# Kernel optimization log

Hardware: AMD Instinct MI355X
Metric: run time of the kernel (lower is better)

Reference implementation:

```python
import jax, jax.numpy as jnp
import numpy as np

B, S, H, NH, HD = 2, 2048, 1024, 16, 64
RD = 16            # rotary_dim = head_dim * 0.25
W = 16             # mini_context_length (sliding window)
SCALE = HD ** -0.5
ROPE_BASE = 10000.0


def setup_inputs() -> dict:
    key = jax.random.key(0)
    ks = jax.random.split(key, 10)
    p = lambda k, shape: (jax.random.normal(k, shape, dtype=jnp.float32) * 0.02)
    return {
        "hidden_states": jax.random.normal(ks[0], (B, S, H), dtype=jnp.float32),
        "Wqkv": p(ks[1], (3 * H, H)), "bqkv": p(ks[2], (3 * H,)),
        "Wqa": p(ks[3], (H, H)),      "bqa": p(ks[4], (H,)),
        "Wka": p(ks[5], (H, H)),      "bka": p(ks[6], (H,)),
        "Wd": p(ks[7], (H, H)),       "bd": p(ks[8], (H,)),
    }


def _rotate_half(x):
    x1, x2 = jnp.split(x, 2, axis=-1)
    return jnp.concatenate([-x2, x1], axis=-1)


def _apply_rope(q, k, seq_len):
    # GPT-NeoX style rotary on the first RD dims. q,k: [B,NH,S,RD]
    inv_freq = 1.0 / (ROPE_BASE ** (jnp.arange(0, RD, 2, dtype=jnp.float32) / RD))
    t = jnp.arange(seq_len, dtype=jnp.float32)
    freqs = jnp.outer(t, inv_freq)                     # [S, RD//2]
    emb = jnp.concatenate([freqs, freqs], axis=-1)     # [S, RD]
    cos = jnp.cos(emb)[None, None]                      # [1,1,S,RD]
    sin = jnp.sin(emb)[None, None]
    return q * cos + _rotate_half(q) * sin, k * cos + _rotate_half(k) * sin


def reference(hidden_states, Wqkv, bqkv, Wqa, bqa, Wka, bka, Wd, bd):
    b, s, _ = hidden_states.shape
    qkv = hidden_states @ Wqkv.T + bqkv                       # [B,S,3H]
    qkv = qkv.reshape(b, s, 3, NH, HD).transpose(2, 0, 3, 1, 4)
    q, k, v = qkv[0], qkv[1], qkv[2]                          # [B,NH,S,HD]

    q_rot, k_rot = _apply_rope(q[..., :RD], k[..., :RD], s)
    q = jnp.concatenate([q_rot, q[..., RD:]], axis=-1)
    k = jnp.concatenate([k_rot, k[..., RD:]], axis=-1)

    # ----- Stage 1: sliding-window local attention (vectorized) -----
    pos = jnp.arange(s)
    idx = pos[:, None] - (W - 1) + jnp.arange(W)[None, :]     # [S,W]
    valid = idx >= 0
    idxc = jnp.clip(idx, 0, s - 1)
    k_win = k[:, :, idxc, :]                                   # [B,NH,S,W,HD]
    v_win = v[:, :, idxc, :]
    scores = jnp.einsum('bhsd,bhswd->bhsw', q, k_win) * SCALE
    scores = jnp.where(valid[None, None], scores, -jnp.inf)
    probs = jax.nn.softmax(scores, axis=-1)
    A = jnp.einsum('bhsw,bhswd->bhsd', probs, v_win)           # [B,NH,S,HD]

    A_hidden = A.transpose(0, 2, 1, 3).reshape(b, s, H)        # [B,S,H]

    # ----- Stage 2: causal global attention over A -----
    qa = (A_hidden @ Wqa.T + bqa).reshape(b, s, NH, HD).transpose(0, 2, 1, 3)
    ka = (A_hidden @ Wka.T + bka).reshape(b, s, NH, HD).transpose(0, 2, 1, 3)
    g = jnp.einsum('bhqd,bhkd->bhqk', qa, ka) * SCALE          # [B,NH,S,S]
    causal = pos[:, None] >= pos[None, :]
    g = jnp.where(causal[None, None], g, -jnp.inf)
    pg = jax.nn.softmax(g, axis=-1)
    out = jnp.einsum('bhqk,bhkd->bhqd', pg, A)                 # [B,NH,S,HD]
    out = out.transpose(0, 2, 1, 3).reshape(b, s, H)
    return out @ Wd.T + bd
```

## Files before the change

### kernel.cpp

```cpp
#include <hip/hip_runtime.h>
#include <hip/hip_bf16.h>
#include <cstdint>
#include <cstddef>

typedef __bf16 bf16;
typedef __bf16 bf16x4 __attribute__((ext_vector_type(4)));
typedef __bf16 bf16x8 __attribute__((ext_vector_type(8)));
typedef float  f32x4  __attribute__((ext_vector_type(4)));

#define DEVINL __device__ __forceinline__

constexpr int   Bc  = 2, Sc = 2048, Hc = 1024, NHc = 16, HDc = 64;
constexpr int   Tc  = Bc * Sc;
constexpr float L2E = 1.44269504088896340736f;
constexpr float NEG_BIG = -1.0e30f;

typedef __attribute__((address_space(1))) void AS1void;
typedef __attribute__((address_space(3))) void AS3void;

DEVINL void load_lds16(const bf16* g, bf16* l) {
  __builtin_amdgcn_global_load_lds((AS1void*)g, (AS3void*)l, 16, 0, 0);
}


__global__ __launch_bounds__(256)
void convert_all(const float* __restrict__ hs, const float* __restrict__ Wqkv,
                 const float* __restrict__ Wqa, const float* __restrict__ Wka,
                 const float* __restrict__ Wd, const float* __restrict__ bqa,
                 const float* __restrict__ bka,
                 bf16* __restrict__ hsb, bf16* __restrict__ wqkvb,
                 bf16* __restrict__ wqakab, bf16* __restrict__ wdb,
                 float* __restrict__ bqaka) {
  const int blk = blockIdx.x;
  if (blk >= 5120) {
    const int i = threadIdx.x * 8;
    const float* src = (i < 1024) ? (bqa + i) : (bka + i - 1024);
    *(f32x4*)(bqaka + i)     = *(const f32x4*)src;
    *(f32x4*)(bqaka + i + 4) = *(const f32x4*)(src + 4);
    return;
  }
  const float* src; bf16* dst; int base;
  if      (blk < 2048) { src = hs;   dst = hsb;                    base = blk; }
  else if (blk < 3584) { src = Wqkv; dst = wqkvb;                  base = blk - 2048; }
  else if (blk < 4096) { src = Wqa;  dst = wqakab;                 base = blk - 3584; }
  else if (blk < 4608) { src = Wka;  dst = wqakab + 1024 * 1024;   base = blk - 4096; }
  else                 { src = Wd;   dst = wdb;                    base = blk - 4608; }
  const int i = (base * 256 + threadIdx.x) * 8;
  f32x4 a = *(const f32x4*)(src + i);
  f32x4 b = *(const f32x4*)(src + i + 4);
  bf16x8 v;
#pragma unroll
  for (int j = 0; j < 4; j++) { v[j] = (bf16)a[j]; v[4 + j] = (bf16)b[j]; }
  *(bf16x8*)(dst + i) = v;
}

template <typename CT>
__global__ __launch_bounds__(256, 3)
void gemm128(const bf16* __restrict__ A, const bf16* __restrict__ Bw,
             const float* __restrict__ bias, CT* __restrict__ C,
             int M, int N, int K) {
  __shared__ __attribute__((aligned(16))) bf16 As[128 * 64];
  __shared__ __attribute__((aligned(16))) bf16 Bs[128 * 64];

  const int tid = threadIdx.x, wv = tid >> 6, lane = tid & 63;
  const int m0 = blockIdx.y * 128, n0 = blockIdx.x * 128;
  const int col = lane & 15, quad = lane >> 4;
  const int wrow = (wv >> 1) * 64, wcol = (wv & 1) * 64;

  f32x4 acc[4][4];
#pragma unroll
  for (int i = 0; i < 4; i++)
#pragma unroll
    for (int j = 0; j < 4; j++) acc[i][j] = f32x4{0.f, 0.f, 0.f, 0.f};

  const int srow = tid >> 3;
  const int scol = (((tid & 7) ^ (srow & 7)) << 3);
  const bf16* Ag = A  + (size_t)(m0 + srow) * K + scol;
  const bf16* Bg = Bw + (size_t)(n0 + srow) * K + scol;
  const int cs = col & 7;

  for (int k0 = 0; k0 < K; k0 += 64) {
#pragma unroll
    for (int c = 0; c < 4; c++) {
      load_lds16(Ag + (size_t)(c * 32) * K + k0, As + c * 2048 + tid * 8);
      load_lds16(Bg + (size_t)(c * 32) * K + k0, Bs + c * 2048 + tid * 8);
    }
    __syncthreads();
#pragma unroll
    for (int kk = 0; kk < 64; kk += 32) {
      const int so = ((((kk >> 3) + quad) ^ cs) << 3);
      bf16x8 af[4], bfr[4];
#pragma unroll
      for (int i = 0; i < 4; i++)
        af[i] = *(const bf16x8*)(As + (wrow + i * 16 + col) * 64 + so);
#pragma unroll
      for (int j = 0; j < 4; j++)
        bfr[j] = *(const bf16x8*)(Bs + (wcol + j * 16 + col) * 64 + so);
#pragma unroll
      for (int i = 0; i < 4; i++)
#pragma unroll
        for (int j = 0; j < 4; j++)
          acc[i][j] = __builtin_amdgcn_mfma_f32_16x16x32_bf16(af[i], bfr[j], acc[i][j], 0, 0, 0);
    }
    __syncthreads();
  }

#pragma unroll
  for (int j = 0; j < 4; j++) {
    const int c = n0 + wcol + j * 16 + col;
    const float bv = bias[c];
#pragma unroll
    for (int i = 0; i < 4; i++)
#pragma unroll
      for (int r = 0; r < 4; r++) {
        const int rr = m0 + wrow + i * 16 + quad * 4 + r;
        C[(size_t)rr * N + c] = (CT)(acc[i][j][r] + bv);
      }
  }
}

template <typename CT>
__global__ __launch_bounds__(256, 4)
void gemm6464(const bf16* __restrict__ A, const bf16* __restrict__ Bw,
              const float* __restrict__ bias, CT* __restrict__ C,
              int M, int N, int K) {
  __shared__ __attribute__((aligned(16))) bf16 As[64 * 64];
  __shared__ __attribute__((aligned(16))) bf16 Bs[64 * 64];

  const int tid = threadIdx.x, wv = tid >> 6, lane = tid & 63;
  const int m0 = blockIdx.y * 64, n0 = blockIdx.x * 64;
  const int col = lane & 15, quad = lane >> 4;

  f32x4 acc[4];
#pragma unroll
  for (int j = 0; j < 4; j++) acc[j] = f32x4{0.f, 0.f, 0.f, 0.f};

  const int srow = tid >> 3;
  const int scol = (((tid & 7) ^ (srow & 7)) << 3);
  const bf16* Ag = A  + (size_t)(m0 + srow) * K + scol;
  const bf16* Bg = Bw + (size_t)(n0 + srow) * K + scol;
  const int cs = col & 7;

  for (int k0 = 0; k0 < K; k0 += 64) {
#pragma unroll
    for (int c = 0; c < 2; c++) {
      load_lds16(Ag + (size_t)(c * 32) * K + k0, As + c * 2048 + tid * 8);
      load_lds16(Bg + (size_t)(c * 32) * K + k0, Bs + c * 2048 + tid * 8);
    }
    __syncthreads();
#pragma unroll
    for (int kk = 0; kk < 64; kk += 32) {
      const int so = ((((kk >> 3) + quad) ^ cs) << 3);
      bf16x8 af = *(const bf16x8*)(As + (wv * 16 + col) * 64 + so);
#pragma unroll
      for (int j = 0; j < 4; j++) {
        bf16x8 bfr = *(const bf16x8*)(Bs + (j * 16 + col) * 64 + so);
        acc[j] = __builtin_amdgcn_mfma_f32_16x16x32_bf16(af, bfr, acc[j], 0, 0, 0);
      }
    }
    __syncthreads();
  }

#pragma unroll
  for (int j = 0; j < 4; j++) {
    const int c = n0 + j * 16 + col;
    const float bv = bias[c];
#pragma unroll
    for (int r = 0; r < 4; r++) {
      const int rr = m0 + wv * 16 + quad * 4 + r;
      C[(size_t)rr * N + c] = (CT)(acc[j][r] + bv);
    }
  }
}

__global__ __launch_bounds__(256)
void window_attn(const bf16* __restrict__ qkv, bf16* __restrict__ Ah,
                 bf16* __restrict__ VTg) {
  __shared__ __attribute__((aligned(16))) bf16 Kw[31 * 72];
  __shared__ __attribute__((aligned(16))) bf16 Vw[31 * 72];
  const int g  = blockIdx.x;
  const int st = g & 127;
  const int h  = (g >> 7) & 15;
  const int b  = g >> 11;
  const int s0 = st * 16;
  const int tid = threadIdx.x;

  if ((tid < 124) || (tid >= 128 && tid < 252)) {
    const bool isK = tid < 124;
    const int lt  = isK ? tid : tid - 128;
    const int r   = lt >> 2, off = (lt & 3) << 4;
    int sidx = s0 - 15 + r; if (sidx < 0) sidx = 0;
    const bf16* src = qkv + (size_t)(b * Sc + sidx) * 3072 + (isK ? 1024 : 2048) + h * 64 + off;
    bf16x8 v0 = *(const bf16x8*)src;
    bf16x8 v1 = *(const bf16x8*)(src + 8);
    if (isK && off == 0) {
#pragma unroll
      for (int j = 0; j < 8; j++) {
        const float invf = exp2f(-(float)j * 1.66096404744368128f);
        float sn, csn;
        sincosf((float)sidx * invf, &sn, &csn);
        const float x1 = (float)v0[j], x2 = (float)v1[j];
        v0[j] = (bf16)(x1 * csn - x2 * sn);
        v1[j] = (bf16)(x2 * csn + x1 * sn);
      }
    }
    bf16* dst = (isK ? Kw : Vw) + r * 72 + off;
    *(bf16x8*)dst       = v0;
    *(bf16x8*)(dst + 8) = v1;
  }
  __syncthreads();

  const int wv = tid >> 6, lane = tid & 63;
  const int subq = lane >> 4, lane16 = lane & 15;
  const int s = s0 + wv * 4 + subq;
  const int t = b * Sc + s;
  const int d0 = lane16 * 4;

  float qd[4];
  {
    bf16x4 qv = *(const bf16x4*)(qkv + (size_t)t * 3072 + h * 64 + d0);
#pragma unroll
    for (int j = 0; j < 4; j++) qd[j] = (float)qv[j];
  }
  float pd[4];
#pragma unroll
  for (int j = 0; j < 4; j++) pd[j] = __shfl_xor(qd[j], 2, 64);
  if (lane16 < 4) {
#pragma unroll
    for (int j = 0; j < 4; j++) {
      const int jabs = d0 + j;
      const float invf = exp2f(-(float)(jabs & 7) * 1.66096404744368128f);
      float sn, csn;
      sincosf((float)s * invf, &sn, &csn);
      qd[j] = (jabs < 8) ? (qd[j] * csn - pd[j] * sn) : (qd[j] * csn + pd[j] * sn);
    }
  }

  float sc[16];
#pragma unroll
  for (int w = 0; w < 16; w++) {
    const int idxp = s - 15 + w;
    const int row = idxp - s0 + 15;
    bf16x4 kv = *(const bf16x4*)(Kw + row * 72 + d0);
    float p = qd[0] * (float)kv[0] + qd[1] * (float)kv[1] +
              qd[2] * (float)kv[2] + qd[3] * (float)kv[3];
#pragma unroll
    for (int m = 1; m < 16; m <<= 1) p += __shfl_xor(p, m, 64);
    sc[w] = (idxp < 0) ? NEG_BIG : p * 0.125f;
  }
  float mx = sc[0];
#pragma unroll
  for (int w = 1; w < 16; w++) mx = fmaxf(mx, sc[w]);
  float sum = 0.f;
#pragma unroll
  for (int w = 0; w < 16; w++) { sc[w] = exp2f((sc[w] - mx) * L2E); sum += sc[w]; }
  const float inv = 1.0f / fmaxf(sum, 1e-30f);

  float acc[4] = {0.f, 0.f, 0.f, 0.f};
#pragma unroll
  for (int w = 0; w < 16; w++) {
    const int idxp = s - 15 + w;
    const int row = idxp - s0 + 15;
    bf16x4 vv = *(const bf16x4*)(Vw + row * 72 + d0);
#pragma unroll
    for (int j = 0; j < 4; j++) acc[j] += sc[w] * (float)vv[j];
  }
  bf16x4 ov;
#pragma unroll
  for (int j = 0; j < 4; j++) ov[j] = (bf16)(acc[j] * inv);
  *(bf16x4*)(Ah + (size_t)t * 1024 + h * 64 + d0) = ov;
  bf16* vt = VTg + (((size_t)(b * 16 + h)) * 64 + d0) * 2048 + s;
#pragma unroll
  for (int j = 0; j < 4; j++) vt[(size_t)j * 2048] = ov[j];
}

__global__ __launch_bounds__(256, 2)
void flash_attn(const bf16* __restrict__ Q, const bf16* __restrict__ Kt,
                const bf16* __restrict__ VTg, bf16* __restrict__ O) {
  constexpr int QS = 2048;
  constexpr float SHIFT = 16.0f;
  __shared__ __attribute__((aligned(16))) bf16 K_lds[2][128 * 64];
  __shared__ __attribute__((aligned(16))) bf16 VT_lds[2][64 * 128];

  const int tid = threadIdx.x, wv = tid >> 6, lane = tid & 63;
  const int bh = blockIdx.x;
  const int y  = blockIdx.y;
  const int qtA = y, qtB = 31 - y;
  const int nA = (qtA + 2) >> 1;
  const int b = bh >> 4, h = bh & 15;
  const int col = lane & 15, quad = lane >> 4;
  const size_t bS = (size_t)b * Sc;
  const int hd = h * 64;

  const int krow = tid >> 3;
  const int kcol = (((tid & 7) ^ (krow & 7)) << 3);
  const int vrow = tid >> 4;
  const int vcol = (((tid & 15) ^ vrow) << 3);
  const int cs8 = col & 7;

  bf16x8 qA0, qA1, qB0, qB1;
  {
    const bf16* qpA = Q + (bS + qtA * 64 + wv * 16 + col) * QS + hd + quad * 8;
    const bf16* qpB = Q + (bS + qtB * 64 + wv * 16 + col) * QS + hd + quad * 8;
    qA0 = *(const bf16x8*)qpA;
    qA1 = *(const bf16x8*)(qpA + 32);
    qB0 = *(const bf16x8*)qpB;
    qB1 = *(const bf16x8*)(qpB + 32);
#pragma unroll
    for (int j = 0; j < 8; j++) {
      qA0[j] = (bf16)((float)qA0[j] * 0.125f);
      qA1[j] = (bf16)((float)qA1[j] * 0.125f);
      qB0[j] = (bf16)((float)qB0[j] * 0.125f);
      qB1[j] = (bf16)((float)qB1[j] * 0.125f);
    }
  }

  auto stage = [&](int bufi, int k0) {
#pragma unroll
    for (int c = 0; c < 4; c++) {
      load_lds16(Kt + (bS + k0 + c * 32 + krow) * QS + hd + kcol,
                 K_lds[bufi] + c * 2048 + tid * 8);
      load_lds16(VTg + ((size_t)bh * 64 + c * 16 + vrow) * 2048 + k0 + vcol,
                 VT_lds[bufi] + c * 2048 + tid * 8);
    }
  };

  f32x4 oacc[4];
#pragma unroll
  for (int i = 0; i < 4; i++) oacc[i] = f32x4{0.f, 0.f, 0.f, 0.f};
  float lsum = 0.f;

  stage(0, 0);
  __syncthreads();
  int cur = 0;

  for (int it = 0; it < 17; it++) {
    const int seg  = (it >= nA);
    const int kt   = seg ? (it - nA) : it;
    const int nkt  = seg ? (17 - nA) : nA;
    const int qt   = seg ? qtB : qtA;
    const int k0   = kt * 128;
    const int qbase = qt * 64 + wv * 16;

    if (it + 1 < 17) {
      const int kt2 = (it + 1 >= nA) ? (it + 1 - nA) : (it + 1);
      stage(cur ^ 1, kt2 * 128);
    }

    bf16x8 q0, q1;
    if (seg == 0) { q0 = qA0; q1 = qA1; } else { q0 = qB0; q1 = qB1; }

    const bf16* Kl = K_lds[cur];
    const bf16* Vl = VT_lds[cur];

    f32x4 sacc[8];
#pragma unroll
    for (int sub = 0; sub < 8; sub++) {
      f32x4 a = f32x4{0.f, 0.f, 0.f, 0.f};
      {
        const int so = ((quad ^ cs8) << 3);
        bf16x8 kf = *(const bf16x8*)(Kl + (sub * 16 + col) * 64 + so);
        a = __builtin_amdgcn_mfma_f32_16x16x32_bf16(kf, q0, a, 0, 0, 0);
      }
      {
        const int so = (((4 + quad) ^ cs8) << 3);
        bf16x8 kf = *(const bf16x8*)(Kl + (sub * 16 + col) * 64 + so);
        a = __builtin_amdgcn_mfma_f32_16x16x32_bf16(kf, q1, a, 0, 0, 0);
      }
      sacc[sub] = a;
    }
    if (kt == nkt - 1) {
      const int qq = qbase + col;
#pragma unroll
      for (int sub = 0; sub < 8; sub++)
#pragma unroll
        for (int r = 0; r < 4; r++) {
          const int key = k0 + sub * 16 + quad * 4 + r;
          if (key > qq) sacc[sub][r] = NEG_BIG;
        }
    }
#pragma unroll
    for (int sub = 0; sub < 8; sub++)
#pragma unroll
      for (int r = 0; r < 4; r++) {
        sacc[sub][r] = exp2f(sacc[sub][r] * L2E - SHIFT);
        lsum += sacc[sub][r];
      }

#pragma unroll
    for (int t = 0; t < 4; t++) {
      uint32_t a0, a1, b0, b1;
      asm("v_cvt_pk_bf16_f32 %0, %1, %2"
          : "=v"(a0) : "v"(sacc[2 * t][0]), "v"(sacc[2 * t][1]));
      asm("v_cvt_pk_bf16_f32 %0, %1, %2"
          : "=v"(a1) : "v"(sacc[2 * t][2]), "v"(sacc[2 * t][3]));
      asm("v_cvt_pk_bf16_f32 %0, %1, %2"
          : "=v"(b0) : "v"(sacc[2 * t + 1][0]), "v"(sacc[2 * t + 1][1]));
      asm("v_cvt_pk_bf16_f32 %0, %1, %2"
          : "=v"(b1) : "v"(sacc[2 * t + 1][2]), "v"(sacc[2 * t + 1][3]));
      asm("v_permlane32_swap_b32 %0, %1" : "+v"(a0), "+v"(b0));
      asm("v_permlane16_swap_b32 %0, %1" : "+v"(a0), "+v"(b0));
      asm("v_permlane32_swap_b32 %0, %1" : "+v"(a1), "+v"(b1));
      asm("v_permlane16_swap_b32 %0, %1" : "+v"(a1), "+v"(b1));
      union { uint32_t u[4]; bf16x8 v; } pk;
      pk.u[0] = a0; pk.u[1] = a1; pk.u[2] = b0; pk.u[3] = b1;
      const int vso = (((4 * t + quad) ^ col) << 3);
#pragma unroll
      for (int nb = 0; nb < 4; nb++) {
        bf16x8 vf = *(const bf16x8*)(Vl + (nb * 16 + col) * 128 + vso);
        oacc[nb] = __builtin_amdgcn_mfma_f32_16x16x32_bf16(pk.v, vf, oacc[nb], 0, 0, 0);
      }
    }

    if (kt == nkt - 1) {
      float tot = lsum;
      tot += __shfl_xor(tot, 16, 64);
      tot += __shfl_xor(tot, 32, 64);
      float lrow[4];
#pragma unroll
      for (int r = 0; r < 4; r++)
        lrow[r] = 1.0f / fmaxf(__shfl(tot, quad * 4 + r, 16), 1e-37f);
#pragma unroll
      for (int nb = 0; nb < 4; nb++)
#pragma unroll
        for (int r = 0; r < 4; r++) {
          const int qq = qbase + quad * 4 + r;
          O[(bS + qq) * 1024 + hd + nb * 16 + col] = (bf16)(oacc[nb][r] * lrow[r]);
        }
#pragma unroll
      for (int i = 0; i < 4; i++) oacc[i] = f32x4{0.f, 0.f, 0.f, 0.f};
      lsum = 0.f;
    }

    __syncthreads();
    cur ^= 1;
  }
}

extern "C" void kernel_launch(void* const* d_in, const int* in_sizes, int n_in,
                              void* d_out, int out_size, void* d_ws, size_t ws_size,
                              hipStream_t stream) {
  (void)in_sizes; (void)n_in; (void)out_size; (void)ws_size;
  const float* hs   = (const float*)d_in[0];
  const float* Wqkv = (const float*)d_in[1];
  const float* bqkv = (const float*)d_in[2];
  const float* Wqa  = (const float*)d_in[3];
  const float* bqa  = (const float*)d_in[4];
  const float* Wka  = (const float*)d_in[5];
  const float* bka  = (const float*)d_in[6];
  const float* Wd   = (const float*)d_in[7];
  const float* bd   = (const float*)d_in[8];
  float* out = (float*)d_out;

  const size_t TH = (size_t)Tc * Hc;
  bf16* dob   = (bf16*)d_out;
  bf16* hsb   = dob;
  bf16* wqkvb = dob + TH;
  bf16* Ah    = dob;
  bf16* VTg   = dob + TH;
  bf16* ws     = (bf16*)d_ws;
  bf16* qkv    = ws;
  bf16* qaka   = ws;
  bf16* oh     = ws + 2 * TH;
  bf16* wqakab = ws + 3 * TH;
  bf16* wdb    = wqakab + 2 * 1024 * 1024;
  float* bqaka = (float*)(wdb + 1024 * 1024);

  convert_all<<<dim3(5121), 256, 0, stream>>>(hs, Wqkv, Wqa, Wka, Wd, bqa, bka,
                                              hsb, wqkvb, wqakab, wdb, bqaka);

  gemm128<bf16><<<dim3(24, 32), 256, 0, stream>>>(hsb, wqkvb, bqkv, qkv, Tc, 3 * Hc, Hc);
  window_attn<<<dim3(Tc * NHc / 16), 256, 0, stream>>>(qkv, Ah, VTg);
  gemm128<bf16><<<dim3(16, 32), 256, 0, stream>>>(Ah, wqakab, bqaka, qaka, Tc, 2 * Hc, Hc);
  flash_attn<<<dim3(Bc * NHc, 16), 256, 0, stream>>>(qaka, qaka + Hc, VTg, oh);
  gemm6464<float><<<dim3(16, 64), 256, 0, stream>>>(oh, wdb, bd, out, Tc, Hc, Hc);
}
```

Baseline: 238.2 us.

## Split key tile across wave pairs in flash attention with LDS reduction

```diff
diff --git a/kernel.cpp b/kernel.cpp
--- a/kernel.cpp
+++ b/kernel.cpp
@@ -274,7 +274,7 @@
   for (int j = 0; j < 4; j++) vt[(size_t)j * 2048] = ov[j];
 }
 
-__global__ __launch_bounds__(256, 2)
+__global__ __launch_bounds__(512, 4)
 void flash_attn(const bf16* __restrict__ Q, const bf16* __restrict__ Kt,
                 const bf16* __restrict__ VTg, bf16* __restrict__ O) {
   constexpr int QS = 2048;
@@ -283,6 +283,7 @@
   __shared__ __attribute__((aligned(16))) bf16 VT_lds[2][64 * 128];
 
   const int tid = threadIdx.x, wv = tid >> 6, lane = tid & 63;
+  const int kw = wv & 1, qw = wv >> 1;
   const int bh = blockIdx.x;
   const int y  = blockIdx.y;
   const int qtA = y, qtB = 31 - y;
@@ -295,13 +296,13 @@
   const int krow = tid >> 3;
   const int kcol = (((tid & 7) ^ (krow & 7)) << 3);
   const int vrow = tid >> 4;
-  const int vcol = (((tid & 15) ^ vrow) << 3);
+  const int vcol = (((tid & 15) ^ (vrow & 15)) << 3);
   const int cs8 = col & 7;
 
   bf16x8 qA0, qA1, qB0, qB1;
   {
-    const bf16* qpA = Q + (bS + qtA * 64 + wv * 16 + col) * QS + hd + quad * 8;
-    const bf16* qpB = Q + (bS + qtB * 64 + wv * 16 + col) * QS + hd + quad * 8;
+    const bf16* qpA = Q + (bS + qtA * 64 + qw * 16 + col) * QS + hd + quad * 8;
+    const bf16* qpB = Q + (bS + qtB * 64 + qw * 16 + col) * QS + hd + quad * 8;
     qA0 = *(const bf16x8*)qpA;
     qA1 = *(const bf16x8*)(qpA + 32);
     qB0 = *(const bf16x8*)qpB;
@@ -317,11 +318,11 @@
 
   auto stage = [&](int bufi, int k0) {
 #pragma unroll
-    for (int c = 0; c < 4; c++) {
-      load_lds16(Kt + (bS + k0 + c * 32 + krow) * QS + hd + kcol,
-                 K_lds[bufi] + c * 2048 + tid * 8);
-      load_lds16(VTg + ((size_t)bh * 64 + c * 16 + vrow) * 2048 + k0 + vcol,
-                 VT_lds[bufi] + c * 2048 + tid * 8);
+    for (int c = 0; c < 2; c++) {
+      load_lds16(Kt + (bS + k0 + c * 64 + krow) * QS + hd + kcol,
+                 K_lds[bufi] + c * 4096 + tid * 8);
+      load_lds16(VTg + ((size_t)bh * 64 + c * 32 + vrow) * 2048 + k0 + vcol,
+                 VT_lds[bufi] + c * 4096 + tid * 8);
     }
   };
 
@@ -340,7 +341,7 @@
     const int nkt  = seg ? (17 - nA) : nA;
     const int qt   = seg ? qtB : qtA;
     const int k0   = kt * 128;
-    const int qbase = qt * 64 + wv * 16;
+    const int qbase = qt * 64 + qw * 16;
 
     if (it + 1 < 17) {
       const int kt2 = (it + 1 >= nA) ? (it + 1 - nA) : (it + 1);
@@ -350,12 +351,12 @@
     bf16x8 q0, q1;
     if (seg == 0) { q0 = qA0; q1 = qA1; } else { q0 = qB0; q1 = qB1; }
 
-    const bf16* Kl = K_lds[cur];
+    const bf16* Kl = K_lds[cur] + kw * 4096;
     const bf16* Vl = VT_lds[cur];
 
-    f32x4 sacc[8];
-#pragma unroll
-    for (int sub = 0; sub < 8; sub++) {
+    f32x4 sacc[4];
+#pragma unroll
+    for (int sub = 0; sub < 4; sub++) {
       f32x4 a = f32x4{0.f, 0.f, 0.f, 0.f};
       {
         const int so = ((quad ^ cs8) << 3);
@@ -372,15 +373,15 @@
     if (kt == nkt - 1) {
       const int qq = qbase + col;
 #pragma unroll
-      for (int sub = 0; sub < 8; sub++)
+      for (int sub = 0; sub < 4; sub++)
 #pragma unroll
         for (int r = 0; r < 4; r++) {
-          const int key = k0 + sub * 16 + quad * 4 + r;
+          const int key = k0 + kw * 64 + sub * 16 + quad * 4 + r;
           if (key > qq) sacc[sub][r] = NEG_BIG;
         }
     }
 #pragma unroll
-    for (int sub = 0; sub < 8; sub++)
+    for (int sub = 0; sub < 4; sub++)
 #pragma unroll
       for (int r = 0; r < 4; r++) {
         sacc[sub][r] = exp2f(sacc[sub][r] * L2E - SHIFT);
@@ -388,7 +389,7 @@
       }
 
 #pragma unroll
-    for (int t = 0; t < 4; t++) {
+    for (int t = 0; t < 2; t++) {
       uint32_t a0, a1, b0, b1;
       asm("v_cvt_pk_bf16_f32 %0, %1, %2"
           : "=v"(a0) : "v"(sacc[2 * t][0]), "v"(sacc[2 * t][1]));
@@ -404,7 +405,7 @@
       asm("v_permlane16_swap_b32 %0, %1" : "+v"(a1), "+v"(b1));
       union { uint32_t u[4]; bf16x8 v; } pk;
       pk.u[0] = a0; pk.u[1] = a1; pk.u[2] = b0; pk.u[3] = b1;
-      const int vso = (((4 * t + quad) ^ col) << 3);
+      const int vso = (((8 * kw + 4 * t + quad) ^ col) << 3);
 #pragma unroll
       for (int nb = 0; nb < 4; nb++) {
         bf16x8 vf = *(const bf16x8*)(Vl + (nb * 16 + col) * 128 + vso);
@@ -413,20 +414,37 @@
     }
 
     if (kt == nkt - 1) {
-      float tot = lsum;
-      tot += __shfl_xor(tot, 16, 64);
-      tot += __shfl_xor(tot, 32, 64);
-      float lrow[4];
-#pragma unroll
-      for (int r = 0; r < 4; r++)
-        lrow[r] = 1.0f / fmaxf(__shfl(tot, quad * 4 + r, 16), 1e-37f);
-#pragma unroll
-      for (int nb = 0; nb < 4; nb++)
-#pragma unroll
-        for (int r = 0; r < 4; r++) {
-          const int qq = qbase + quad * 4 + r;
-          O[(bS + qq) * 1024 + hd + nb * 16 + col] = (bf16)(oacc[nb][r] * lrow[r]);
-        }
+      __syncthreads();
+      float* scr = (qw < 2) ? (float*)(&K_lds[cur][0]) + ((qw * 64) + lane) * 17
+                            : (float*)(&VT_lds[cur][0]) + (((qw - 2) * 64) + lane) * 17;
+      if (kw == 1) {
+#pragma unroll
+        for (int nb = 0; nb < 4; nb++)
+#pragma unroll
+          for (int r = 0; r < 4; r++) scr[nb * 4 + r] = oacc[nb][r];
+        scr[16] = lsum;
+      }
+      __syncthreads();
+      if (kw == 0) {
+#pragma unroll
+        for (int nb = 0; nb < 4; nb++)
+#pragma unroll
+          for (int r = 0; r < 4; r++) oacc[nb][r] += scr[nb * 4 + r];
+        float tot = lsum + scr[16];
+        tot += __shfl_xor(tot, 16, 64);
+        tot += __shfl_xor(tot, 32, 64);
+        float lrow[4];
+#pragma unroll
+        for (int r = 0; r < 4; r++)
+          lrow[r] = 1.0f / fmaxf(__shfl(tot, quad * 4 + r, 16), 1e-37f);
+#pragma unroll
+        for (int nb = 0; nb < 4; nb++)
+#pragma unroll
+          for (int r = 0; r < 4; r++) {
+            const int qq = qbase + quad * 4 + r;
+            O[(bS + qq) * 1024 + hd + nb * 16 + col] = (bf16)(oacc[nb][r] * lrow[r]);
+          }
+      }
 #pragma unroll
       for (int i = 0; i < 4; i++) oacc[i] = f32x4{0.f, 0.f, 0.f, 0.f};
       lsum = 0.f;
@@ -472,6 +490,6 @@
   gemm128<bf16><<<dim3(24, 32), 256, 0, stream>>>(hsb, wqkvb, bqkv, qkv, Tc, 3 * Hc, Hc);
   window_attn<<<dim3(Tc * NHc / 16), 256, 0, stream>>>(qkv, Ah, VTg);
   gemm128<bf16><<<dim3(16, 32), 256, 0, stream>>>(Ah, wqakab, bqaka, qaka, Tc, 2 * Hc, Hc);
-  flash_attn<<<dim3(Bc * NHc, 16), 256, 0, stream>>>(qaka, qaka + Hc, VTg, oh);
+  flash_attn<<<dim3(Bc * NHc, 16), 512, 0, stream>>>(qaka, qaka + Hc, VTg, oh);
   gemm6464<float><<<dim3(16, 64), 256, 0, stream>>>(oh, wdb, bd, out, Tc, Hc, Hc);
 }
```

Result: no change. 238.9 us (+0.3%).

## Triple-buffer flash attention with 512-thread blocks and 128-row query tiles

Applied to the files above, without the earlier changes.

```diff
diff --git a/kernel.cpp b/kernel.cpp
--- a/kernel.cpp
+++ b/kernel.cpp
@@ -21,6 +21,12 @@
 DEVINL void load_lds16(const bf16* g, bf16* l) {
   __builtin_amdgcn_global_load_lds((AS1void*)g, (AS3void*)l, 16, 0, 0);
 }
+
+#if __has_builtin(__builtin_amdgcn_exp2f)
+DEVINL float fast_exp2(float x) { return __builtin_amdgcn_exp2f(x); }
+#else
+DEVINL float fast_exp2(float x) { return exp2f(x); }
+#endif
 
 
 __global__ __launch_bounds__(256)
@@ -274,56 +280,59 @@
   for (int j = 0; j < 4; j++) vt[(size_t)j * 2048] = ov[j];
 }
 
-__global__ __launch_bounds__(256, 2)
+__global__ __launch_bounds__(512, 2)
 void flash_attn(const bf16* __restrict__ Q, const bf16* __restrict__ Kt,
                 const bf16* __restrict__ VTg, bf16* __restrict__ O) {
   constexpr int QS = 2048;
-  constexpr float SHIFT = 16.0f;
-  __shared__ __attribute__((aligned(16))) bf16 K_lds[2][128 * 64];
-  __shared__ __attribute__((aligned(16))) bf16 VT_lds[2][64 * 128];
+  __shared__ __attribute__((aligned(16))) bf16 K_lds[3][128 * 64];
+  __shared__ __attribute__((aligned(16))) bf16 VT_lds[3][64 * 128];
 
   const int tid = threadIdx.x, wv = tid >> 6, lane = tid & 63;
   const int bh = blockIdx.x;
   const int y  = blockIdx.y;
-  const int qtA = y, qtB = 31 - y;
-  const int nA = (qtA + 2) >> 1;
+  const int qtA = y, qtB = 15 - y;
+  const int nA = y + 1;
   const int b = bh >> 4, h = bh & 15;
   const int col = lane & 15, quad = lane >> 4;
   const size_t bS = (size_t)b * Sc;
   const int hd = h * 64;
+  const int cs8 = col & 7;
 
   const int krow = tid >> 3;
-  const int kcol = (((tid & 7) ^ (krow & 7)) << 3);
+  const int kswz = (((tid & 7) ^ (krow & 7)) << 3);
   const int vrow = tid >> 4;
-  const int vcol = (((tid & 15) ^ vrow) << 3);
-  const int cs8 = col & 7;
+  const int vswz = (((tid & 15) ^ (vrow & 15)) << 3);
+  const bf16* Kg0 = Kt  + (bS * QS) + (size_t)krow * QS + hd + kswz;
+  const bf16* Vg0 = VTg + ((size_t)bh * 64 + vrow) * 2048 + vswz;
 
   bf16x8 qA0, qA1, qB0, qB1;
   {
-    const bf16* qpA = Q + (bS + qtA * 64 + wv * 16 + col) * QS + hd + quad * 8;
-    const bf16* qpB = Q + (bS + qtB * 64 + wv * 16 + col) * QS + hd + quad * 8;
+    constexpr float QSC = 0.125f * L2E;
+    const bf16* qpA = Q + (bS + qtA * 128 + wv * 16 + col) * QS + hd + quad * 8;
+    const bf16* qpB = Q + (bS + qtB * 128 + wv * 16 + col) * QS + hd + quad * 8;
     qA0 = *(const bf16x8*)qpA;
     qA1 = *(const bf16x8*)(qpA + 32);
     qB0 = *(const bf16x8*)qpB;
     qB1 = *(const bf16x8*)(qpB + 32);
 #pragma unroll
     for (int j = 0; j < 8; j++) {
-      qA0[j] = (bf16)((float)qA0[j] * 0.125f);
-      qA1[j] = (bf16)((float)qA1[j] * 0.125f);
-      qB0[j] = (bf16)((float)qB0[j] * 0.125f);
-      qB1[j] = (bf16)((float)qB1[j] * 0.125f);
+      qA0[j] = (bf16)((float)qA0[j] * QSC);
+      qA1[j] = (bf16)((float)qA1[j] * QSC);
+      qB0[j] = (bf16)((float)qB0[j] * QSC);
+      qB1[j] = (bf16)((float)qB1[j] * QSC);
     }
   }
 
   auto stage = [&](int bufi, int k0) {
-#pragma unroll
-    for (int c = 0; c < 4; c++) {
-      load_lds16(Kt + (bS + k0 + c * 32 + krow) * QS + hd + kcol,
-                 K_lds[bufi] + c * 2048 + tid * 8);
-      load_lds16(VTg + ((size_t)bh * 64 + c * 16 + vrow) * 2048 + k0 + vcol,
-                 VT_lds[bufi] + c * 2048 + tid * 8);
+    const bf16* kg = Kg0 + (size_t)k0 * QS;
+    const bf16* vg = Vg0 + k0;
+#pragma unroll
+    for (int c = 0; c < 2; c++) {
+      load_lds16(kg + (size_t)(c * 64) * QS, K_lds[bufi] + c * 4096 + tid * 8);
+      load_lds16(vg + (size_t)(c * 32) * 2048, VT_lds[bufi] + c * 4096 + tid * 8);
     }
   };
+  auto k0of = [&](int i) { return ((i >= nA) ? i - nA : i) * 128; };
 
   f32x4 oacc[4];
 #pragma unroll
@@ -331,8 +340,7 @@
   float lsum = 0.f;
 
   stage(0, 0);
-  __syncthreads();
-  int cur = 0;
+  stage(1, k0of(1));
 
   for (int it = 0; it < 17; it++) {
     const int seg  = (it >= nA);
@@ -340,20 +348,25 @@
     const int nkt  = seg ? (17 - nA) : nA;
     const int qt   = seg ? qtB : qtA;
     const int k0   = kt * 128;
-    const int qbase = qt * 64 + wv * 16;
-
-    if (it + 1 < 17) {
-      const int kt2 = (it + 1 >= nA) ? (it + 1 - nA) : (it + 1);
-      stage(cur ^ 1, kt2 * 128);
-    }
+    const int qbase = qt * 128 + wv * 16;
+    const int bufc = it % 3;
+
+    if (it == 16)                      asm volatile("s_waitcnt vmcnt(0)" ::: "memory");
+    else if (it == nA || it == nA + 1) asm volatile("s_waitcnt vmcnt(20)" ::: "memory");
+    else                               asm volatile("s_waitcnt vmcnt(4)" ::: "memory");
+    __builtin_amdgcn_s_barrier();
+    __builtin_amdgcn_sched_barrier(0);
+
+    if (it + 2 < 17) stage((it + 2) % 3, k0of(it + 2));
 
     bf16x8 q0, q1;
-    if (seg == 0) { q0 = qA0; q1 = qA1; } else { q0 = qB0; q1 = qB1; }
-
-    const bf16* Kl = K_lds[cur];
-    const bf16* Vl = VT_lds[cur];
+    if (seg) { q0 = qB0; q1 = qB1; } else { q0 = qA0; q1 = qA1; }
+
+    const bf16* Kl = K_lds[bufc];
+    const bf16* Vl = VT_lds[bufc];
 
     f32x4 sacc[8];
+    __builtin_amdgcn_s_setprio(1);
 #pragma unroll
     for (int sub = 0; sub < 8; sub++) {
       f32x4 a = f32x4{0.f, 0.f, 0.f, 0.f};
@@ -369,6 +382,8 @@
       }
       sacc[sub] = a;
     }
+    __builtin_amdgcn_s_setprio(0);
+
     if (kt == nkt - 1) {
       const int qq = qbase + col;
 #pragma unroll
@@ -383,8 +398,9 @@
     for (int sub = 0; sub < 8; sub++)
 #pragma unroll
       for (int r = 0; r < 4; r++) {
-        sacc[sub][r] = exp2f(sacc[sub][r] * L2E - SHIFT);
-        lsum += sacc[sub][r];
+        const float p = fast_exp2(sacc[sub][r]);
+        sacc[sub][r] = p;
+        lsum += p;
       }
 
 #pragma unroll
@@ -405,11 +421,13 @@
       union { uint32_t u[4]; bf16x8 v; } pk;
       pk.u[0] = a0; pk.u[1] = a1; pk.u[2] = b0; pk.u[3] = b1;
       const int vso = (((4 * t + quad) ^ col) << 3);
+      __builtin_amdgcn_s_setprio(1);
 #pragma unroll
       for (int nb = 0; nb < 4; nb++) {
         bf16x8 vf = *(const bf16x8*)(Vl + (nb * 16 + col) * 128 + vso);
         oacc[nb] = __builtin_amdgcn_mfma_f32_16x16x32_bf16(pk.v, vf, oacc[nb], 0, 0, 0);
       }
+      __builtin_amdgcn_s_setprio(0);
     }
 
     if (kt == nkt - 1) {
@@ -431,9 +449,6 @@
       for (int i = 0; i < 4; i++) oacc[i] = f32x4{0.f, 0.f, 0.f, 0.f};
       lsum = 0.f;
     }
-
-    __syncthreads();
-    cur ^= 1;
   }
 }
 
@@ -472,6 +487,6 @@
   gemm128<bf16><<<dim3(24, 32), 256, 0, stream>>>(hsb, wqkvb, bqkv, qkv, Tc, 3 * Hc, Hc);
   window_attn<<<dim3(Tc * NHc / 16), 256, 0, stream>>>(qkv, Ah, VTg);
   gemm128<bf16><<<dim3(16, 32), 256, 0, stream>>>(Ah, wqakab, bqaka, qaka, Tc, 2 * Hc, Hc);
-  flash_attn<<<dim3(Bc * NHc, 16), 256, 0, stream>>>(qaka, qaka + Hc, VTg, oh);
+  flash_attn<<<dim3(Bc * NHc, 8), 512, 0, stream>>>(qaka, qaka + Hc, VTg, oh);
   gemm6464<float><<<dim3(16, 64), 256, 0, stream>>>(oh, wdb, bd, out, Tc, Hc, Hc);
 }
```

Result: faster. 226.7 us (-4.8%).
